# Kernel optimization log

Measured on AMD Instinct MI355X. Metric: run time of the kernel, lower is better.

## Reference

```python
import jax, jax.numpy as jnp
import numpy as np

EPS = 1e-5


def setup_inputs() -> dict:
    key = jax.random.key(0)
    ks = jax.random.split(key, 5)
    N, E, D, L = 10000, 160000, 512, 3
    x = jax.random.normal(ks[0], (N, D), dtype=jnp.float32)
    src = jax.random.randint(ks[1], (E,), 0, N, dtype=jnp.int64)
    dst = jax.random.randint(ks[2], (E,), 0, N, dtype=jnp.int64)
    gamma = jnp.ones((L, D), dtype=jnp.float32)
    beta = jnp.zeros((L, D), dtype=jnp.float32)
    # glorot-ish scale so ReLU stack stays well-conditioned
    W = jax.random.normal(ks[3], (L, D, D), dtype=jnp.float32) * (1.0 / np.sqrt(D))
    b = jnp.zeros((L, D), dtype=jnp.float32)
    return {"x": x, "src": src, "dst": dst, "gamma": gamma, "beta": beta, "W": W, "b": b}


def reference(x, src, dst, gamma, beta, W, b):
    N = x.shape[0]
    ones = jnp.ones(src.shape[0], dtype=x.dtype)
    # DGL GraphConv norm='both': src side uses out-degree, dst side uses in-degree
    out_deg = jnp.clip(jax.ops.segment_sum(ones, src, num_segments=N), 1.0)
    in_deg = jnp.clip(jax.ops.segment_sum(ones, dst, num_segments=N), 1.0)
    src_norm = (out_deg ** -0.5)[:, None]  # [N,1]
    dst_norm = (in_deg ** -0.5)[:, None]   # [N,1]
    n_layers = gamma.shape[0]
    for i in range(n_layers):
        # BatchNorm1d (training mode: batch mean, biased variance)
        mu = jnp.mean(x, axis=0)
        var = jnp.var(x, axis=0)
        x = (x - mu) * jax.lax.rsqrt(var + EPS) * gamma[i] + beta[i]
        h = x * src_norm
        agg = jax.ops.segment_sum(h[src], dst, num_segments=N) * dst_norm
        x = jax.nn.relu(agg @ W[i] + b[i])
    return x
```

## Files before the change

### kernel.cpp

```cpp
#include <hip/hip_runtime.h>
#include <hip/hip_bf16.h>

constexpr int N = 10000;
constexpr int D = 512;
constexpr int E = 160000;
constexpr int L = 3;
constexpr float EPS = 1e-5f;

typedef _Float16 half8 __attribute__((ext_vector_type(8)));
typedef _Float16 half2v __attribute__((ext_vector_type(2)));
typedef float floatx4 __attribute__((ext_vector_type(4)));

__device__ __forceinline__ void glds16(const _Float16* g, _Float16* l) {
    __builtin_amdgcn_global_load_lds(
        (const __attribute__((address_space(1))) uint32_t*)(g),
        (__attribute__((address_space(3))) uint32_t*)(l),
        16, 0, 0);
}

constexpr int DEG_BLOCKS  = (E + 255) / 256;
constexpr int CONV_BLOCKS = 100;
constexpr int TW_BLOCKS   = L * 256;
constexpr int MEGA_BLOCKS = DEG_BLOCKS + CONV_BLOCKS + TW_BLOCKS;

__global__ __launch_bounds__(256) void mega_setup(
    const int* __restrict__ src, const int* __restrict__ dst,
    const float* __restrict__ x, const float* __restrict__ W,
    int* __restrict__ out_deg, int* __restrict__ in_deg,
    _Float16* __restrict__ x16, float* __restrict__ stats0,
    _Float16* __restrict__ Wt) {
    __shared__ float tb[32][33];
    int bid = blockIdx.x;
    int tid = threadIdx.x;
    if (bid < DEG_BLOCKS) {
        int e = bid * 256 + tid;
        if (e < E) {
            atomicAdd(&out_deg[src[e]], 1);
            atomicAdd(&in_deg[dst[e]], 1);
        }
    } else if (bid < DEG_BLOCKS + CONV_BLOCKS) {
        int b = bid - DEG_BLOCKS;
        int r0 = b * 100;
        int r1 = r0 + 100; if (r1 > N) r1 = N;
        int c2 = tid * 2;
        float s0 = 0.f, s1 = 0.f, q0 = 0.f, q1 = 0.f;
        for (int r = r0; r < r1; ++r) {
            float2 v = *(const float2*)(x + (size_t)r * D + c2);
            s0 += v.x; q0 += v.x * v.x;
            s1 += v.y; q1 += v.y * v.y;
            half2v h; h[0] = (_Float16)v.x; h[1] = (_Float16)v.y;
            *(half2v*)(x16 + (size_t)r * D + c2) = h;
        }
        atomicAdd(&stats0[c2], s0);
        atomicAdd(&stats0[c2 + 1], s1);
        atomicAdd(&stats0[D + c2], q0);
        atomicAdd(&stats0[D + c2 + 1], q1);
    } else {
        int b = bid - DEG_BLOCKS - CONV_BLOCKS;
        int l = b >> 8;
        int t = b & 255;
        int k0 = (t >> 4) * 32, n0 = (t & 15) * 32;
        int tx = tid & 31, ty = tid >> 5;
        const float* Wl = W + (size_t)l * D * D;
        _Float16* Wtl = Wt + (size_t)l * D * D;
        for (int i = 0; i < 32; i += 8)
            tb[ty + i][tx] = Wl[(size_t)(k0 + ty + i) * D + n0 + tx];
        __syncthreads();
        for (int i = 0; i < 32; i += 8)
            Wtl[(size_t)(n0 + ty + i) * D + k0 + tx] = (_Float16)tb[tx][ty + i];
    }
}

__global__ void scan_indeg(const int* __restrict__ in_deg,
                           const int* __restrict__ out_deg,
                           int* __restrict__ off, int* __restrict__ cursor,
                           float* __restrict__ src_norm, float* __restrict__ dst_norm) {
    __shared__ int lsum[1024];
    int t = threadIdx.x;
    const int chunk = (N + 1023) / 1024;
    int start = t * chunk;
    int end = start + chunk; if (end > N) end = N;
    int s = 0;
    for (int i = start; i < end; ++i) s += in_deg[i];
    lsum[t] = s;
    __syncthreads();
    for (int d = 1; d < 1024; d <<= 1) {
        int v = (t >= d) ? lsum[t - d] : 0;
        __syncthreads();
        lsum[t] += v;
        __syncthreads();
    }
    int excl = (t == 0) ? 0 : lsum[t - 1];
    for (int i = start; i < end; ++i) {
        off[i] = excl;
        cursor[i] = excl;
        excl += in_deg[i];
        int od = out_deg[i]; if (od < 1) od = 1;
        int id = in_deg[i];  if (id < 1) id = 1;
        src_norm[i] = rsqrtf((float)od);
        dst_norm[i] = rsqrtf((float)id);
    }
    if (t == 1023) off[N] = lsum[1023];
}

__global__ void csr_fill(const int* __restrict__ src, const int* __restrict__ dst,
                         int* __restrict__ cursor, int* __restrict__ csr_src) {
    int e = blockIdx.x * blockDim.x + threadIdx.x;
    if (e >= E) return;
    int d = dst[e];
    int pos = atomicAdd(&cursor[d], 1);
    csr_src[pos] = src[e];
}

__global__ __launch_bounds__(256) void aggregate_bn(
    const _Float16* __restrict__ x, const int* __restrict__ off,
    const int* __restrict__ csr_src, const float* __restrict__ src_norm,
    const float* __restrict__ dst_norm, const float* __restrict__ stats,
    const float* __restrict__ gamma, const float* __restrict__ beta,
    _Float16* __restrict__ agg) {
    int wid = (blockIdx.x * 256 + threadIdx.x) >> 6;
    if (wid >= N) return;
    int lane = threadIdx.x & 63;
    int c0 = lane * 8;

    float scale[8], shift[8];
    const float invN = 1.0f / (float)N;
    for (int i = 0; i < 8; ++i) {
        int c = c0 + i;
        float mu = stats[c] * invN;
        float var = stats[D + c] * invN - mu * mu;
        float sc = gamma[c] * rsqrtf(var + EPS);
        scale[i] = sc;
        shift[i] = beta[c] - mu * sc;
    }

    int e0 = off[wid], e1 = off[wid + 1];
    float a[8] = {}, a2[8] = {};
    float t = 0.f;
    int e = e0;
    for (; e + 2 <= e1; e += 2) {
        int s0 = csr_src[e];
        int s1 = csr_src[e + 1];
        float n0 = src_norm[s0];
        float n1 = src_norm[s1];
        half8 v0 = *(const half8*)(x + (size_t)s0 * D + c0);
        half8 v1 = *(const half8*)(x + (size_t)s1 * D + c0);
        t += n0 + n1;
        for (int i = 0; i < 8; ++i) {
            a[i]  += (float)v0[i] * n0;
            a2[i] += (float)v1[i] * n1;
        }
    }
    if (e < e1) {
        int s0 = csr_src[e];
        float n0 = src_norm[s0];
        half8 v0 = *(const half8*)(x + (size_t)s0 * D + c0);
        t += n0;
        for (int i = 0; i < 8; ++i) a[i] += (float)v0[i] * n0;
    }
    float dn = dst_norm[wid];
    half8 o;
    for (int i = 0; i < 8; ++i)
        o[i] = (_Float16)(dn * (scale[i] * (a[i] + a2[i]) + shift[i] * t));
    *(half8*)(agg + (size_t)wid * D + c0) = o;
}

template <typename OutT, bool STATS>
__global__ __launch_bounds__(256) void mm_f16_relu(
    const _Float16* __restrict__ A, const _Float16* __restrict__ Bt,
    const float* __restrict__ bias, OutT* __restrict__ C, int M,
    float* __restrict__ stats) {
    __shared__ __align__(16) _Float16 As[128 * 32];
    __shared__ __align__(16) _Float16 Bs[64 * 32];
    const int tid  = threadIdx.x;
    const int wave = tid >> 6;
    const int lane = tid & 63;
    const int quad = lane >> 4;
    const int l16  = lane & 15;
    const int row0 = blockIdx.x * 128;
    const int col0 = blockIdx.y * 64;
    const int wm = (wave & 1) * 64;
    const int wn = (wave >> 1) * 32;
    const int sr = lane >> 2;
    const int sc = (lane & 3) * 8;

    int ar0 = row0 + wave * 32 + sr;
    int ar1 = ar0 + 16;
    if (ar0 >= M) ar0 = M - 1;
    if (ar1 >= M) ar1 = M - 1;
    const _Float16* gA0 = A + (size_t)ar0 * D + sc;
    const _Float16* gA1 = A + (size_t)ar1 * D + sc;
    const _Float16* gB  = Bt + (size_t)(col0 + wave * 16 + sr) * D + sc;
    _Float16* lA0 = As + (wave * 32) * 32;
    _Float16* lA1 = As + (wave * 32 + 16) * 32;
    _Float16* lB  = Bs + (wave * 16) * 32;

    floatx4 acc[4][2] = {};

    for (int k0 = 0; k0 < D; k0 += 32) {
        __syncthreads();
        glds16(gA0 + k0, lA0);
        glds16(gA1 + k0, lA1);
        glds16(gB + k0, lB);
        __syncthreads();
        half8 af[4], bf[2];
        for (int i = 0; i < 4; ++i)
            af[i] = *(const half8*)(As + (wm + i * 16 + l16) * 32 + quad * 8);
        for (int j = 0; j < 2; ++j)
            bf[j] = *(const half8*)(Bs + (wn + j * 16 + l16) * 32 + quad * 8);
        for (int i = 0; i < 4; ++i)
            for (int j = 0; j < 2; ++j)
                acc[i][j] = __builtin_amdgcn_mfma_f32_16x16x32_f16(af[i], bf[j], acc[i][j], 0, 0, 0);
    }

    float s[2] = {}, q[2] = {};
    for (int i = 0; i < 4; ++i) {
        for (int r = 0; r < 4; ++r) {
            int row = row0 + wm + i * 16 + quad * 4 + r;
            bool valid = row < M;
            for (int j = 0; j < 2; ++j) {
                int col = col0 + wn + j * 16 + l16;
                float v = acc[i][j][r] + bias[col];
                v = v > 0.f ? v : 0.f;
                if (valid) {
                    C[(size_t)row * D + col] = (OutT)v;
                    if (STATS) { s[j] += v; q[j] += v * v; }
                }
            }
        }
    }
    if (STATS) {
        for (int j = 0; j < 2; ++j) {
            float sv = s[j], qv = q[j];
            sv += __shfl_xor(sv, 16); sv += __shfl_xor(sv, 32);
            qv += __shfl_xor(qv, 16); qv += __shfl_xor(qv, 32);
            if (quad == 0) {
                int col = col0 + wn + j * 16 + l16;
                atomicAdd(&stats[col], sv);
                atomicAdd(&stats[D + col], qv);
            }
        }
    }
}

extern "C" void kernel_launch(void* const* d_in, const int* in_sizes, int n_in,
                              void* d_out, int out_size, void* d_ws, size_t ws_size,
                              hipStream_t stream) {
    const float* x_in  = (const float*)d_in[0];
    const int*   src   = (const int*)d_in[1];
    const int*   dst   = (const int*)d_in[2];
    const float* gamma = (const float*)d_in[3];
    const float* beta  = (const float*)d_in[4];
    const float* W     = (const float*)d_in[5];
    const float* b     = (const float*)d_in[6];
    float* out = (float*)d_out;

    char* p = (char*)d_ws;
    _Float16* x16 = (_Float16*)p;  p += (size_t)N * D * 2;
    _Float16* agg = (_Float16*)p;  p += (size_t)N * D * 2;
    _Float16* Wt  = (_Float16*)p;  p += (size_t)L * D * D * 2;
    float* src_norm = (float*)p;   p += (size_t)N * 4;
    float* dst_norm = (float*)p;   p += (size_t)N * 4;
    int* out_deg   = (int*)p;      p += (size_t)N * 4;
    int* in_deg    = (int*)p;      p += (size_t)N * 4;
    float* stats0  = (float*)p;    p += 2 * D * 4;
    float* stats1  = (float*)p;    p += 2 * D * 4;
    float* stats2  = (float*)p;    p += 2 * D * 4;
    int* csr_off   = (int*)p;      p += (size_t)(N + 1) * 4;
    int* cursor    = (int*)p;      p += (size_t)N * 4;
    int* csr_src   = (int*)p;      p += (size_t)E * 4;

    float* stats_in[3] = {stats0, stats1, stats2};

    hipMemsetAsync(out_deg, 0, (2 * (size_t)N + 6 * D) * sizeof(int), stream);
    mega_setup<<<MEGA_BLOCKS, 256, 0, stream>>>(src, dst, x_in, W,
                                                out_deg, in_deg, x16, stats0, Wt);
    scan_indeg<<<1, 1024, 0, stream>>>(in_deg, out_deg, csr_off, cursor,
                                       src_norm, dst_norm);
    csr_fill<<<DEG_BLOCKS, 256, 0, stream>>>(src, dst, cursor, csr_src);

    dim3 mm_grid((N + 127) / 128, D / 64);
    const int agg_blocks = (N + 3) / 4;

    for (int l = 0; l < L; ++l) {
        const float* gl  = gamma + (size_t)l * D;
        const float* bl  = beta + (size_t)l * D;
        const _Float16* Wl = Wt + (size_t)l * D * D;
        const float* bil = b + (size_t)l * D;

        aggregate_bn<<<agg_blocks, 256, 0, stream>>>(
            x16, csr_off, csr_src, src_norm, dst_norm, stats_in[l], gl, bl, agg);
        if (l == L - 1) {
            mm_f16_relu<float, false><<<mm_grid, 256, 0, stream>>>(
                agg, Wl, bil, out, N, nullptr);
        } else {
            mm_f16_relu<_Float16, true><<<mm_grid, 256, 0, stream>>>(
                agg, Wl, bil, x16, N, stats_in[l + 1]);
        }
    }
}
```

Before: 282.5 us.

## Fuse aggregation+BN with GEMM per 16-row block, ping-pong activation buffers

Merges the per-layer aggregate_bn and tiled MFMA GEMM kernels into one fused_layer kernel. Each 256-thread block aggregates 16 destination rows into LDS and then multiplies them by the full 512-column weight, with B fragments read straight from global memory. This removes the agg buffer's write and re-read and half the launches per layer, and adds ping-pong x buffers because the layer can no longer write its input in place. In exchange every block re-reads the whole 512x512 weight matrix from global/L2, and MFMA reuse drops to a single 16-row A tile per wave.

```diff
diff --git a/kernel.cpp b/kernel.cpp
--- a/kernel.cpp
+++ b/kernel.cpp
@@ -10,13 +10,6 @@
 typedef _Float16 half8 __attribute__((ext_vector_type(8)));
 typedef _Float16 half2v __attribute__((ext_vector_type(2)));
 typedef float floatx4 __attribute__((ext_vector_type(4)));
-
-__device__ __forceinline__ void glds16(const _Float16* g, _Float16* l) {
-    __builtin_amdgcn_global_load_lds(
-        (const __attribute__((address_space(1))) uint32_t*)(g),
-        (__attribute__((address_space(3))) uint32_t*)(l),
-        16, 0, 0);
-}
 
 constexpr int DEG_BLOCKS  = (E + 255) / 256;
 constexpr int CONV_BLOCKS = 100;
@@ -112,132 +105,104 @@
     csr_src[pos] = src[e];
 }
 
-__global__ __launch_bounds__(256) void aggregate_bn(
-    const _Float16* __restrict__ x, const int* __restrict__ off,
+constexpr int RP = 520;
+
+template <typename OutT, bool STATS>
+__global__ __launch_bounds__(256) void fused_layer(
+    const _Float16* __restrict__ xin, const int* __restrict__ off,
     const int* __restrict__ csr_src, const float* __restrict__ src_norm,
-    const float* __restrict__ dst_norm, const float* __restrict__ stats,
+    const float* __restrict__ dst_norm, const float* __restrict__ stats_in,
     const float* __restrict__ gamma, const float* __restrict__ beta,
-    _Float16* __restrict__ agg) {
-    int wid = (blockIdx.x * 256 + threadIdx.x) >> 6;
-    if (wid >= N) return;
-    int lane = threadIdx.x & 63;
-    int c0 = lane * 8;
-
-    float scale[8], shift[8];
-    const float invN = 1.0f / (float)N;
-    for (int i = 0; i < 8; ++i) {
-        int c = c0 + i;
-        float mu = stats[c] * invN;
-        float var = stats[D + c] * invN - mu * mu;
-        float sc = gamma[c] * rsqrtf(var + EPS);
-        scale[i] = sc;
-        shift[i] = beta[c] - mu * sc;
-    }
-
-    int e0 = off[wid], e1 = off[wid + 1];
-    float a[8] = {}, a2[8] = {};
-    float t = 0.f;
-    int e = e0;
-    for (; e + 2 <= e1; e += 2) {
-        int s0 = csr_src[e];
-        int s1 = csr_src[e + 1];
-        float n0 = src_norm[s0];
-        float n1 = src_norm[s1];
-        half8 v0 = *(const half8*)(x + (size_t)s0 * D + c0);
-        half8 v1 = *(const half8*)(x + (size_t)s1 * D + c0);
-        t += n0 + n1;
-        for (int i = 0; i < 8; ++i) {
-            a[i]  += (float)v0[i] * n0;
-            a2[i] += (float)v1[i] * n1;
-        }
-    }
-    if (e < e1) {
-        int s0 = csr_src[e];
-        float n0 = src_norm[s0];
-        half8 v0 = *(const half8*)(x + (size_t)s0 * D + c0);
-        t += n0;
-        for (int i = 0; i < 8; ++i) a[i] += (float)v0[i] * n0;
-    }
-    float dn = dst_norm[wid];
-    half8 o;
-    for (int i = 0; i < 8; ++i)
-        o[i] = (_Float16)(dn * (scale[i] * (a[i] + a2[i]) + shift[i] * t));
-    *(half8*)(agg + (size_t)wid * D + c0) = o;
-}
-
-template <typename OutT, bool STATS>
-__global__ __launch_bounds__(256) void mm_f16_relu(
-    const _Float16* __restrict__ A, const _Float16* __restrict__ Bt,
-    const float* __restrict__ bias, OutT* __restrict__ C, int M,
-    float* __restrict__ stats) {
-    __shared__ __align__(16) _Float16 As[128 * 32];
-    __shared__ __align__(16) _Float16 Bs[64 * 32];
+    const _Float16* __restrict__ Bt, const float* __restrict__ bias,
+    OutT* __restrict__ Cout, float* __restrict__ stats_out) {
+    __shared__ __align__(16) _Float16 As[16 * RP];
     const int tid  = threadIdx.x;
     const int wave = tid >> 6;
     const int lane = tid & 63;
     const int quad = lane >> 4;
     const int l16  = lane & 15;
-    const int row0 = blockIdx.x * 128;
-    const int col0 = blockIdx.y * 64;
-    const int wm = (wave & 1) * 64;
-    const int wn = (wave >> 1) * 32;
-    const int sr = lane >> 2;
-    const int sc = (lane & 3) * 8;
-
-    int ar0 = row0 + wave * 32 + sr;
-    int ar1 = ar0 + 16;
-    if (ar0 >= M) ar0 = M - 1;
-    if (ar1 >= M) ar1 = M - 1;
-    const _Float16* gA0 = A + (size_t)ar0 * D + sc;
-    const _Float16* gA1 = A + (size_t)ar1 * D + sc;
-    const _Float16* gB  = Bt + (size_t)(col0 + wave * 16 + sr) * D + sc;
-    _Float16* lA0 = As + (wave * 32) * 32;
-    _Float16* lA1 = As + (wave * 32 + 16) * 32;
-    _Float16* lB  = Bs + (wave * 16) * 32;
-
-    floatx4 acc[4][2] = {};
-
+    const int row_base = blockIdx.x * 16;
+    const int c0 = lane * 8;
+
+    float scale[8], shift[8];
+    const float invN = 1.0f / (float)N;
+    for (int i = 0; i < 8; ++i) {
+        int c = c0 + i;
+        float mu = stats_in[c] * invN;
+        float var = stats_in[D + c] * invN - mu * mu;
+        float sc = gamma[c] * rsqrtf(var + EPS);
+        scale[i] = sc;
+        shift[i] = beta[c] - mu * sc;
+    }
+
+    for (int i = 0; i < 4; ++i) {
+        int r = wave * 4 + i;
+        int n = row_base + r;
+        int e0 = off[n], e1 = off[n + 1];
+        float a[8] = {}, a2[8] = {};
+        float t = 0.f;
+        int e = e0;
+        for (; e + 2 <= e1; e += 2) {
+            int s0 = csr_src[e];
+            int s1 = csr_src[e + 1];
+            float n0 = src_norm[s0];
+            float n1 = src_norm[s1];
+            half8 v0 = *(const half8*)(xin + (size_t)s0 * D + c0);
+            half8 v1 = *(const half8*)(xin + (size_t)s1 * D + c0);
+            t += n0 + n1;
+            for (int k = 0; k < 8; ++k) {
+                a[k]  += (float)v0[k] * n0;
+                a2[k] += (float)v1[k] * n1;
+            }
+        }
+        if (e < e1) {
+            int s0 = csr_src[e];
+            float n0 = src_norm[s0];
+            half8 v0 = *(const half8*)(xin + (size_t)s0 * D + c0);
+            t += n0;
+            for (int k = 0; k < 8; ++k) a[k] += (float)v0[k] * n0;
+        }
+        float dn = dst_norm[n];
+        half8 o;
+        for (int k = 0; k < 8; ++k)
+            o[k] = (_Float16)(dn * (scale[k] * (a[k] + a2[k]) + shift[k] * t));
+        *(half8*)(As + r * RP + c0) = o;
+    }
+    __syncthreads();
+
+    const int colw = wave * 128;
+    floatx4 acc[8] = {};
+    #pragma unroll
     for (int k0 = 0; k0 < D; k0 += 32) {
-        __syncthreads();
-        glds16(gA0 + k0, lA0);
-        glds16(gA1 + k0, lA1);
-        glds16(gB + k0, lB);
-        __syncthreads();
-        half8 af[4], bf[2];
-        for (int i = 0; i < 4; ++i)
-            af[i] = *(const half8*)(As + (wm + i * 16 + l16) * 32 + quad * 8);
-        for (int j = 0; j < 2; ++j)
-            bf[j] = *(const half8*)(Bs + (wn + j * 16 + l16) * 32 + quad * 8);
-        for (int i = 0; i < 4; ++i)
-            for (int j = 0; j < 2; ++j)
-                acc[i][j] = __builtin_amdgcn_mfma_f32_16x16x32_f16(af[i], bf[j], acc[i][j], 0, 0, 0);
-    }
-
-    float s[2] = {}, q[2] = {};
-    for (int i = 0; i < 4; ++i) {
+        half8 af = *(const half8*)(As + l16 * RP + k0 + quad * 8);
+        #pragma unroll
+        for (int j = 0; j < 8; ++j) {
+            half8 bf = *(const half8*)(Bt + (size_t)(colw + j * 16 + l16) * D + k0 + quad * 8);
+            acc[j] = __builtin_amdgcn_mfma_f32_16x16x32_f16(af, bf, acc[j], 0, 0, 0);
+        }
+    }
+
+    float s[8] = {}, q[8] = {};
+    for (int j = 0; j < 8; ++j) {
+        int col = colw + j * 16 + l16;
+        float bi = bias[col];
         for (int r = 0; r < 4; ++r) {
-            int row = row0 + wm + i * 16 + quad * 4 + r;
-            bool valid = row < M;
-            for (int j = 0; j < 2; ++j) {
-                int col = col0 + wn + j * 16 + l16;
-                float v = acc[i][j][r] + bias[col];
-                v = v > 0.f ? v : 0.f;
-                if (valid) {
-                    C[(size_t)row * D + col] = (OutT)v;
-                    if (STATS) { s[j] += v; q[j] += v * v; }
-                }
-            }
+            int row = row_base + quad * 4 + r;
+            float v = acc[j][r] + bi;
+            v = v > 0.f ? v : 0.f;
+            Cout[(size_t)row * D + col] = (OutT)v;
+            if (STATS) { s[j] += v; q[j] += v * v; }
         }
     }
     if (STATS) {
-        for (int j = 0; j < 2; ++j) {
+        for (int j = 0; j < 8; ++j) {
             float sv = s[j], qv = q[j];
             sv += __shfl_xor(sv, 16); sv += __shfl_xor(sv, 32);
             qv += __shfl_xor(qv, 16); qv += __shfl_xor(qv, 32);
             if (quad == 0) {
-                int col = col0 + wn + j * 16 + l16;
-                atomicAdd(&stats[col], sv);
-                atomicAdd(&stats[D + col], qv);
+                int col = colw + j * 16 + l16;
+                atomicAdd(&stats_out[col], sv);
+                atomicAdd(&stats_out[D + col], qv);
             }
         }
     }
@@ -256,9 +221,9 @@
     float* out = (float*)d_out;
 
     char* p = (char*)d_ws;
-    _Float16* x16 = (_Float16*)p;  p += (size_t)N * D * 2;
-    _Float16* agg = (_Float16*)p;  p += (size_t)N * D * 2;
-    _Float16* Wt  = (_Float16*)p;  p += (size_t)L * D * D * 2;
+    _Float16* x16a = (_Float16*)p; p += (size_t)N * D * 2;
+    _Float16* x16b = (_Float16*)p; p += (size_t)N * D * 2;
+    _Float16* Wt   = (_Float16*)p; p += (size_t)L * D * D * 2;
     float* src_norm = (float*)p;   p += (size_t)N * 4;
     float* dst_norm = (float*)p;   p += (size_t)N * 4;
     int* out_deg   = (int*)p;      p += (size_t)N * 4;
@@ -270,32 +235,22 @@
     int* cursor    = (int*)p;      p += (size_t)N * 4;
     int* csr_src   = (int*)p;      p += (size_t)E * 4;
 
-    float* stats_in[3] = {stats0, stats1, stats2};
-
     hipMemsetAsync(out_deg, 0, (2 * (size_t)N + 6 * D) * sizeof(int), stream);
     mega_setup<<<MEGA_BLOCKS, 256, 0, stream>>>(src, dst, x_in, W,
-                                                out_deg, in_deg, x16, stats0, Wt);
+                                                out_deg, in_deg, x16a, stats0, Wt);
     scan_indeg<<<1, 1024, 0, stream>>>(in_deg, out_deg, csr_off, cursor,
                                        src_norm, dst_norm);
     csr_fill<<<DEG_BLOCKS, 256, 0, stream>>>(src, dst, cursor, csr_src);
 
-    dim3 mm_grid((N + 127) / 128, D / 64);
-    const int agg_blocks = (N + 3) / 4;
-
-    for (int l = 0; l < L; ++l) {
-        const float* gl  = gamma + (size_t)l * D;
-        const float* bl  = beta + (size_t)l * D;
-        const _Float16* Wl = Wt + (size_t)l * D * D;
-        const float* bil = b + (size_t)l * D;
-
-        aggregate_bn<<<agg_blocks, 256, 0, stream>>>(
-            x16, csr_off, csr_src, src_norm, dst_norm, stats_in[l], gl, bl, agg);
-        if (l == L - 1) {
-            mm_f16_relu<float, false><<<mm_grid, 256, 0, stream>>>(
-                agg, Wl, bil, out, N, nullptr);
-        } else {
-            mm_f16_relu<_Float16, true><<<mm_grid, 256, 0, stream>>>(
-                agg, Wl, bil, x16, N, stats_in[l + 1]);
-        }
-    }
-}
+    const int blocks = N / 16;
+
+    fused_layer<_Float16, true><<<blocks, 256, 0, stream>>>(
+        x16a, csr_off, csr_src, src_norm, dst_norm, stats0,
+        gamma, beta, Wt, b, x16b, stats1);
+    fused_layer<_Float16, true><<<blocks, 256, 0, stream>>>(
+        x16b, csr_off, csr_src, src_norm, dst_norm, stats1,
+        gamma + D, beta + D, Wt + (size_t)D * D, b + D, x16a, stats2);
+    fused_layer<float, false><<<blocks, 256, 0, stream>>>(
+        x16a, csr_off, csr_src, src_norm, dst_norm, stats2,
+        gamma + 2 * D, beta + 2 * D, Wt + 2 * (size_t)D * D, b + 2 * D, out, nullptr);
+}
```

Measured after the change: 366.1 us. 1.3x slower.

## Widen GEMM tile to 128x128 and unroll gather loop by four

Applied to the files above, without the earlier changes.

The matmul kernel's N-tile doubles from 64 to 128 columns, so each wave computes a 64x64 sub-tile with 16 MFMA accumulators and B loads are split across two LDS rows per wave. The goal is more reuse of the A tile per load and fewer total blocks. The aggregation gather loop now processes four neighbors per iteration instead of two, putting more independent loads in flight. The trade-off is higher register pressure and a grid of 316 GEMM blocks instead of 632, which may leave the device with poorer occupancy and load balance.

```diff
diff --git a/kernel.cpp b/kernel.cpp
--- a/kernel.cpp
+++ b/kernel.cpp
@@ -138,25 +138,33 @@
     float a[8] = {}, a2[8] = {};
     float t = 0.f;
     int e = e0;
-    for (; e + 2 <= e1; e += 2) {
+    for (; e + 4 <= e1; e += 4) {
         int s0 = csr_src[e];
         int s1 = csr_src[e + 1];
+        int s2 = csr_src[e + 2];
+        int s3 = csr_src[e + 3];
         float n0 = src_norm[s0];
         float n1 = src_norm[s1];
+        float n2 = src_norm[s2];
+        float n3 = src_norm[s3];
         half8 v0 = *(const half8*)(x + (size_t)s0 * D + c0);
         half8 v1 = *(const half8*)(x + (size_t)s1 * D + c0);
-        t += n0 + n1;
-        for (int i = 0; i < 8; ++i) {
-            a[i]  += (float)v0[i] * n0;
-            a2[i] += (float)v1[i] * n1;
-        }
-    }
-    if (e < e1) {
+        half8 v2 = *(const half8*)(x + (size_t)s2 * D + c0);
+        half8 v3 = *(const half8*)(x + (size_t)s3 * D + c0);
+        t += (n0 + n1) + (n2 + n3);
+        for (int k = 0; k < 8; ++k) {
+            a[k]  += (float)v0[k] * n0;
+            a2[k] += (float)v1[k] * n1;
+            a[k]  += (float)v2[k] * n2;
+            a2[k] += (float)v3[k] * n3;
+        }
+    }
+    for (; e < e1; ++e) {
         int s0 = csr_src[e];
         float n0 = src_norm[s0];
         half8 v0 = *(const half8*)(x + (size_t)s0 * D + c0);
         t += n0;
-        for (int i = 0; i < 8; ++i) a[i] += (float)v0[i] * n0;
+        for (int k = 0; k < 8; ++k) a[k] += (float)v0[k] * n0;
     }
     float dn = dst_norm[wid];
     half8 o;
@@ -171,16 +179,16 @@
     const float* __restrict__ bias, OutT* __restrict__ C, int M,
     float* __restrict__ stats) {
     __shared__ __align__(16) _Float16 As[128 * 32];
-    __shared__ __align__(16) _Float16 Bs[64 * 32];
+    __shared__ __align__(16) _Float16 Bs[128 * 32];
     const int tid  = threadIdx.x;
     const int wave = tid >> 6;
     const int lane = tid & 63;
     const int quad = lane >> 4;
     const int l16  = lane & 15;
     const int row0 = blockIdx.x * 128;
-    const int col0 = blockIdx.y * 64;
+    const int col0 = blockIdx.y * 128;
     const int wm = (wave & 1) * 64;
-    const int wn = (wave >> 1) * 32;
+    const int wn = (wave >> 1) * 64;
     const int sr = lane >> 2;
     const int sc = (lane & 3) * 8;
 
@@ -190,35 +198,39 @@
     if (ar1 >= M) ar1 = M - 1;
     const _Float16* gA0 = A + (size_t)ar0 * D + sc;
     const _Float16* gA1 = A + (size_t)ar1 * D + sc;
-    const _Float16* gB  = Bt + (size_t)(col0 + wave * 16 + sr) * D + sc;
+    const _Float16* gB0 = Bt + (size_t)(col0 + wave * 32 + sr) * D + sc;
+    const _Float16* gB1 = Bt + (size_t)(col0 + wave * 32 + 16 + sr) * D + sc;
     _Float16* lA0 = As + (wave * 32) * 32;
     _Float16* lA1 = As + (wave * 32 + 16) * 32;
-    _Float16* lB  = Bs + (wave * 16) * 32;
-
-    floatx4 acc[4][2] = {};
+    _Float16* lB0 = Bs + (wave * 32) * 32;
+    _Float16* lB1 = Bs + (wave * 32 + 16) * 32;
+
+    floatx4 acc[4][4] = {};
 
     for (int k0 = 0; k0 < D; k0 += 32) {
         __syncthreads();
         glds16(gA0 + k0, lA0);
         glds16(gA1 + k0, lA1);
-        glds16(gB + k0, lB);
-        __syncthreads();
-        half8 af[4], bf[2];
+        glds16(gB0 + k0, lB0);
+        glds16(gB1 + k0, lB1);
+        __syncthreads();
+        half8 af[4], bf[4];
         for (int i = 0; i < 4; ++i)
             af[i] = *(const half8*)(As + (wm + i * 16 + l16) * 32 + quad * 8);
-        for (int j = 0; j < 2; ++j)
+        for (int j = 0; j < 4; ++j)
             bf[j] = *(const half8*)(Bs + (wn + j * 16 + l16) * 32 + quad * 8);
         for (int i = 0; i < 4; ++i)
-            for (int j = 0; j < 2; ++j)
-                acc[i][j] = __builtin_amdgcn_mfma_f32_16x16x32_f16(af[i], bf[j], acc[i][j], 0, 0, 0);
-    }
-
-    float s[2] = {}, q[2] = {};
+            for (int j = 0; j < 4; ++j)
+                acc[i][j] = __builtin_amdgcn_mfma_f32_16x16x32_f16(
+                    af[i], bf[j], acc[i][j], 0, 0, 0);
+    }
+
+    float s[4] = {}, q[4] = {};
     for (int i = 0; i < 4; ++i) {
         for (int r = 0; r < 4; ++r) {
             int row = row0 + wm + i * 16 + quad * 4 + r;
             bool valid = row < M;
-            for (int j = 0; j < 2; ++j) {
+            for (int j = 0; j < 4; ++j) {
                 int col = col0 + wn + j * 16 + l16;
                 float v = acc[i][j][r] + bias[col];
                 v = v > 0.f ? v : 0.f;
@@ -230,7 +242,7 @@
         }
     }
     if (STATS) {
-        for (int j = 0; j < 2; ++j) {
+        for (int j = 0; j < 4; ++j) {
             float sv = s[j], qv = q[j];
             sv += __shfl_xor(sv, 16); sv += __shfl_xor(sv, 32);
             qv += __shfl_xor(qv, 16); qv += __shfl_xor(qv, 32);
@@ -279,7 +291,7 @@
                                        src_norm, dst_norm);
     csr_fill<<<DEG_BLOCKS, 256, 0, stream>>>(src, dst, cursor, csr_src);
 
-    dim3 mm_grid((N + 127) / 128, D / 64);
+    dim3 mm_grid((N + 127) / 128, D / 128);
     const int agg_blocks = (N + 3) / 4;
 
     for (int l = 0; l < L; ++l) {
```

Result: no change. 281.4 us (-0.4%).
